# Optimization experiments

Measured on AMD Instinct MI355X. Metric: run time of the kernel, lower is better.

The kernel has to match this reference:

```python
import jax, jax.numpy as jnp
import numpy as np

N_NODES, N_EDGES, N_GRAPHS = 5000, 80000, 64
LATENT, HID, STEPS = 128, 512, 3


def _mlp(h, Ws, bs):
    # MLP: ReLU after every linear (incl. last) -- MLPwoLastAct is the variant without it
    for W, b in zip(Ws, bs):
        h = jax.nn.relu(h @ W + b)
    return h


def _mlp_wo_last_act(h, Ws, bs):
    n = len(Ws)
    for i, (W, b) in enumerate(zip(Ws, bs)):
        h = h @ W + b
        if i < n - 1:
            h = jax.nn.relu(h)
    return h


def setup_inputs() -> dict:
    key = jax.random.key(0)
    ks = iter(jax.random.split(key, 64))

    def nrm(shape, s=0.05):
        return (jax.random.normal(next(ks), shape) * s).astype(jnp.float32)

    inp = {}
    inp["x"] = jax.random.normal(next(ks), (N_NODES, LATENT), jnp.float32)
    inp["edge_index"] = jax.random.randint(next(ks), (2, N_EDGES), 0, N_NODES, jnp.int32)
    inp["edge_attr"] = jax.random.normal(next(ks), (N_EDGES, LATENT), jnp.float32)
    inp["u"] = jax.random.normal(next(ks), (N_GRAPHS, LATENT), jnp.float32)
    inp["node_batch"] = jnp.sort(jax.random.randint(next(ks), (N_NODES,), 0, N_GRAPHS, jnp.int32))
    inp["edge_batch"] = jnp.sort(jax.random.randint(next(ks), (N_EDGES,), 0, N_GRAPHS, jnp.int32))
    inp["pos"] = jax.random.normal(next(ks), (N_NODES, 3), jnp.float32)
    inp["last_pos_init"] = jax.random.uniform(next(ks), (N_NODES, 3), jnp.float32, -1.0, 1.0)

    # PosEmbeddingwithMask: pos MLP(3->128->128), dis MLP(1->128->128)
    inp["pos_emb_W1"], inp["pos_emb_b1"] = nrm((3, LATENT)), nrm((LATENT,))
    inp["pos_emb_W2"], inp["pos_emb_b2"] = nrm((LATENT, LATENT)), nrm((LATENT,))
    inp["dis_W1"], inp["dis_b1"] = nrm((1, LATENT)), nrm((LATENT,))
    inp["dis_W2"], inp["dis_b2"] = nrm((LATENT, LATENT)), nrm((LATENT,))

    # per-layer edge / node MLPs: (4*latent) -> 512 -> 512 -> 128, stacked over STEPS
    cin = 4 * LATENT
    for pre in ("edge", "node"):
        inp[f"{pre}_W1"], inp[f"{pre}_b1"] = nrm((STEPS, cin, HID)), nrm((STEPS, HID))
        inp[f"{pre}_W2"], inp[f"{pre}_b2"] = nrm((STEPS, HID, HID)), nrm((STEPS, HID))
        inp[f"{pre}_W3"], inp[f"{pre}_b3"] = nrm((STEPS, HID, LATENT)), nrm((STEPS, LATENT))

    # global MLP only for layers 0..STEPS-2: (3*latent) -> 512 -> 512 -> 128
    gL, gin = STEPS - 1, 3 * LATENT
    inp["glob_W1"], inp["glob_b1"] = nrm((gL, gin, HID)), nrm((gL, HID))
    inp["glob_W2"], inp["glob_b2"] = nrm((gL, HID, HID)), nrm((gL, HID))
    inp["glob_W3"], inp["glob_b3"] = nrm((gL, HID, LATENT)), nrm((gL, LATENT))

    # shared pos_decoder: MLPwoLastAct(128 -> 128 -> 3)
    inp["dec_W1"], inp["dec_b1"] = nrm((LATENT, LATENT)), nrm((LATENT,))
    inp["dec_W2"], inp["dec_b2"] = nrm((LATENT, 3)), nrm((3,))
    return inp


def reference(x, edge_index, edge_attr, u, node_batch, edge_batch, pos, last_pos_init,
              pos_emb_W1, pos_emb_b1, pos_emb_W2, pos_emb_b2,
              dis_W1, dis_b1, dis_W2, dis_b2,
              edge_W1, edge_b1, edge_W2, edge_b2, edge_W3, edge_b3,
              node_W1, node_b1, node_W2, node_b2, node_W3, node_b3,
              glob_W1, glob_b1, glob_W2, glob_b2, glob_W3, glob_b3,
              dec_W1, dec_b1, dec_W2, dec_b2):
    src, dst = edge_index[0], edge_index[1]
    N = x.shape[0]
    counts = jnp.maximum(
        jax.ops.segment_sum(jnp.ones((N, 1), x.dtype), node_batch, N_GRAPHS), 1.0)

    def move2origin(p):
        mean = jax.ops.segment_sum(p, node_batch, N_GRAPHS) / counts
        return p - mean[node_batch]

    xs, es, us = x, edge_attr, u
    last_pos = last_pos_init  # pos_new_zeros.uniform_(-1, 1), materialized as input
    pos_preds = []
    for l in range(STEPS):
        p = last_pos  # mode='mol2conf': pos = last_pred
        # PosEmbeddingwithMask
        ex = xs + _mlp(p, (pos_emb_W1, pos_emb_W2), (pos_emb_b1, pos_emb_b2))
        length = jnp.linalg.norm(p[src] - p[dst], axis=-1, keepdims=True)  # [E,1]
        ee = es + _mlp(length, (dis_W1, dis_W2), (dis_b1, dis_b2))
        # edge update: gather -> MLP
        edge_in = jnp.concatenate([ex[src], ex[dst], ee, us[edge_batch]], axis=-1)
        e1 = _mlp(edge_in, (edge_W1[l], edge_W2[l], edge_W3[l]),
                  (edge_b1[l], edge_b2[l], edge_b3[l]))
        # scatter-reduce (sum) to nodes, then node MLP
        sent = jax.ops.segment_sum(e1, src, N)
        recv = jax.ops.segment_sum(e1, dst, N)
        node_in = jnp.concatenate([ex, sent, recv, us[node_batch]], axis=-1)
        x1 = _mlp(node_in, (node_W1[l], node_W2[l], node_W3[l]),
                  (node_b1[l], node_b2[l], node_b3[l]))
        # global update (None on last layer)
        if l < STEPS - 1:
            g_in = jnp.concatenate([us,
                                    jax.ops.segment_sum(x1, node_batch, N_GRAPHS),
                                    jax.ops.segment_sum(e1, edge_batch, N_GRAPHS)], axis=-1)
            u1 = _mlp(g_in, (glob_W1[l], glob_W2[l], glob_W3[l]),
                      (glob_b1[l], glob_b2[l], glob_b3[l]))
        else:
            u1 = us
        # residuals (dropout is identity in eval)
        xs, es, us = x1 + xs, e1 + es, u1 + us
        # pred_pos_residual=True
        delta = _mlp_wo_last_act(xs, (dec_W1, dec_W2), (dec_b1, dec_b2))
        last_pos = move2origin(last_pos + delta)
        pos_preds.append(last_pos)
    return xs, es, us, jnp.stack(pos_preds)
```

## Files before the change

### kernel.cpp

```cpp
#include <hip/hip_runtime.h>
#include <hip/hip_bf16.h>
#include <stdint.h>

#define NN 5000
#define NE 80000
#define NG 64
#define LAT 128
#define HIDN 512

typedef __hip_bfloat16 bf16;
typedef short short8 __attribute__((ext_vector_type(8)));
typedef float f32x4 __attribute__((ext_vector_type(4)));

__device__ __forceinline__ float b2f(bf16 v) { return __bfloat162float(v); }
__device__ __forceinline__ bf16 f2b(float v) { return __float2bfloat16(v); }
__device__ __forceinline__ short f2bs(float v) {
    bf16 b = __float2bfloat16(v);
    short s; __builtin_memcpy(&s, &b, 2); return s;
}

template<int MODE>
__global__ __launch_bounds__(256, 4)
void gemm64_kernel(const bf16* __restrict__ A, const bf16* __restrict__ Bt,
                   const float* __restrict__ bias,
                   const float* residf, const bf16* residb,
                   float* out_sf, bf16* out_sb, bf16* out_rb,
                   int M, int N, int nnt,
                   const int* __restrict__ g_src, const int* __restrict__ g_dst,
                   const int* __restrict__ g_eb,
                   const bf16* __restrict__ g_ex, const bf16* __restrict__ g_ee,
                   const bf16* __restrict__ g_us)
{
    constexpr int K = 512, NT = K / 64;
    __shared__ __align__(16) char lds[24576];

    const int tid  = threadIdx.x;
    const int lane = tid & 63;
    const int w    = tid >> 6;
    const int li   = lane & 15, grp = lane >> 4;
    const int wr   = w >> 1, wc = w & 1;

    const int nb  = gridDim.x;
    const int q   = nb >> 3, r = nb & 7;
    const int xcd = blockIdx.x & 7, jj = blockIdx.x >> 3;
    const int wg  = (xcd < r ? xcd * (q + 1) : r * (q + 1) + (xcd - r) * q) + jj;
    const int m0  = (wg / nnt) * 128;
    const int n0  = (wg % nnt) * 64;

    f32x4 acc[4][2];
#pragma unroll
    for (int m = 0; m < 4; ++m)
#pragma unroll
        for (int n = 0; n < 2; ++n)
            acc[m][n] = (f32x4){0.f, 0.f, 0.f, 0.f};

    int he[4], hs[4], hd[4], hb[4];
    if (MODE == 1) {
#pragma unroll
        for (int c = 0; c < 4; ++c) {
            const int p  = (tid + c * 256) * 16;
            const int qb = p ^ ((p >> 3) & 0x70);
            int e = m0 + (qb >> 7); if (e >= M) e = M - 1;
            he[c] = e;
            hs[c] = g_src[e]; hd[c] = g_dst[e]; hb[c] = g_eb[e];
        }
    }

    char* ldsA = lds;
    char* ldsB = lds + 16384;

    for (int t = 0; t < NT; ++t) {
#pragma unroll
        for (int c = 0; c < 4; ++c) {
            const int p  = (tid + c * 256) * 16;
            const int qb = p ^ ((p >> 3) & 0x70);
            const int row = qb >> 7;
            const int kk  = (qb & 127) >> 1;
            const bf16* srcp;
            if (MODE == 1) {
                const int seg = t >> 1;
                const int so  = ((t & 1) << 6) + kk;
                if (seg == 0)      srcp = g_ex + (size_t)hs[c] * LAT + so;
                else if (seg == 1) srcp = g_ex + (size_t)hd[c] * LAT + so;
                else if (seg == 2) srcp = g_ee + (size_t)he[c] * LAT + so;
                else               srcp = g_us + (size_t)hb[c] * LAT + so;
            } else {
                int rr = m0 + row; if (rr >= M) rr = M - 1;
                srcp = A + (size_t)rr * K + t * 64 + kk;
            }
            __builtin_amdgcn_global_load_lds(
                (__attribute__((address_space(1))) const void*)srcp,
                (__attribute__((address_space(3))) void*)(ldsA + p), 16, 0, 0);
        }
#pragma unroll
        for (int c = 0; c < 2; ++c) {
            const int p  = (tid + c * 256) * 16;
            const int qb = p ^ ((p >> 3) & 0x70);
            const int row = qb >> 7;
            const int kk  = (qb & 127) >> 1;
            const bf16* srcp = Bt + (size_t)(n0 + row) * K + t * 64 + kk;
            __builtin_amdgcn_global_load_lds(
                (__attribute__((address_space(1))) const void*)srcp,
                (__attribute__((address_space(3))) void*)(ldsB + p), 16, 0, 0);
        }
        __syncthreads();

        short8 af[4][2], bf[2][2];
#pragma unroll
        for (int m = 0; m < 4; ++m) {
            const int row = wr * 64 + m * 16 + li;
            const int xr  = (row & 7) << 4;
#pragma unroll
            for (int s = 0; s < 2; ++s)
                af[m][s] = *(const short8*)(ldsA +
                    ((row * 128 + s * 64 + grp * 16) ^ xr));
        }
#pragma unroll
        for (int n = 0; n < 2; ++n) {
            const int row = wc * 32 + n * 16 + li;
            const int xr  = (row & 7) << 4;
#pragma unroll
            for (int s = 0; s < 2; ++s)
                bf[n][s] = *(const short8*)(ldsB +
                    ((row * 128 + s * 64 + grp * 16) ^ xr));
        }
#pragma unroll
        for (int m = 0; m < 4; ++m)
#pragma unroll
            for (int n = 0; n < 2; ++n)
#pragma unroll
                for (int s = 0; s < 2; ++s)
                    acc[m][n] = __builtin_amdgcn_mfma_f32_16x16x32_bf16(
                        af[m][s], bf[n][s], acc[m][n], 0, 0, 0);
        __syncthreads();
    }

#pragma unroll
    for (int m = 0; m < 4; ++m) {
        const int growb = m0 + wr * 64 + m * 16 + grp * 4;
#pragma unroll
        for (int n = 0; n < 2; ++n) {
            const int gcol = n0 + wc * 32 + n * 16 + li;
            const float bv = bias[gcol];
#pragma unroll
            for (int j = 0; j < 4; ++j) {
                const int grow = growb + j;
                if (grow >= M) continue;
                float val = fmaxf(acc[m][n][j] + bv, 0.f);
                const size_t oo = (size_t)grow * N + gcol;
                if (out_rb) out_rb[oo] = f2b(val);
                float sum = val;
                if (residf) sum += residf[oo];
                if (residb) sum += b2f(residb[oo]);
                if (out_sf) out_sf[oo] = sum;
                if (out_sb) out_sb[oo] = f2b(sum);
            }
        }
    }
}

__global__ __launch_bounds__(256, 4)
void posdis_kernel(int nP,
                   const float* __restrict__ lp,
                   const int* __restrict__ src, const int* __restrict__ dst,
                   const bf16* __restrict__ pBt, const float* __restrict__ pb2v,
                   const float* __restrict__ pW1v, const float* __restrict__ pb1v,
                   const float* __restrict__ xs, bf16* __restrict__ exb,
                   const bf16* __restrict__ dBt, const float* __restrict__ db2v,
                   const float* __restrict__ dW1v, const float* __restrict__ db1v,
                   const bf16* __restrict__ esb, bf16* __restrict__ eeb)
{
    constexpr int K = 128;
    __shared__ __align__(16) bf16 Bs[64 * 32];
    const int tid  = threadIdx.x;
    const int lane = tid & 63;
    const int w    = tid >> 6;
    const int li   = lane & 15, grp = lane >> 4;
    const int wr   = w >> 1, wc = w & 1;

    const bool isP = (int)blockIdx.x < nP;
    const int bid  = isP ? blockIdx.x : blockIdx.x - nP;
    const int M    = isP ? NN : NE;
    const int m0   = (bid >> 1) * 128;
    const int n0   = (bid & 1) * 64;
    const bf16*  Bt   = isP ? pBt  : dBt;
    const float* bias = isP ? pb2v : db2v;
    const float* aW   = isP ? pW1v : dW1v;
    const float* ab   = isP ? pb1v : db1v;

    f32x4 acc[4][2];
#pragma unroll
    for (int m = 0; m < 4; ++m)
#pragma unroll
        for (int n = 0; n < 2; ++n)
            acc[m][n] = (f32x4){0.f, 0.f, 0.f, 0.f};

    float r0[4], r1[4], r2[4];
#pragma unroll
    for (int m = 0; m < 4; ++m) {
        int rr = m0 + wr * 64 + m * 16 + li; if (rr >= M) rr = M - 1;
        if (isP) {
            r0[m] = lp[rr * 3 + 0]; r1[m] = lp[rr * 3 + 1]; r2[m] = lp[rr * 3 + 2];
        } else {
            const int s = src[rr], d = dst[rr];
            const float dx = lp[s*3+0] - lp[d*3+0];
            const float dy = lp[s*3+1] - lp[d*3+1];
            const float dz = lp[s*3+2] - lp[d*3+2];
            r0[m] = sqrtf(dx*dx + dy*dy + dz*dz);
        }
    }

    for (int kt = 0; kt < K / 32; ++kt) {
        {
            const int off = tid * 16;
            const int rr_ = off >> 6;
            const int g   = (off >> 4) & 3;
            const int gl  = g ^ ((rr_ >> 1) & 3);
            const bf16* srcp = Bt + (size_t)(n0 + rr_) * K + kt * 32 + gl * 8;
            __builtin_amdgcn_global_load_lds(
                (__attribute__((address_space(1))) const void*)srcp,
                (__attribute__((address_space(3))) void*)((char*)Bs + off),
                16, 0, 0);
        }
        __syncthreads();

        const int kk0 = kt * 32 + grp * 8;
        float bb[8], w0[8], w1[8], w2[8];
        *(f32x4*)&bb[0] = *(const f32x4*)(ab + kk0);
        *(f32x4*)&bb[4] = *(const f32x4*)(ab + kk0 + 4);
        *(f32x4*)&w0[0] = *(const f32x4*)(aW + kk0);
        *(f32x4*)&w0[4] = *(const f32x4*)(aW + kk0 + 4);
        if (isP) {
            *(f32x4*)&w1[0] = *(const f32x4*)(aW + K + kk0);
            *(f32x4*)&w1[4] = *(const f32x4*)(aW + K + kk0 + 4);
            *(f32x4*)&w2[0] = *(const f32x4*)(aW + 2 * K + kk0);
            *(f32x4*)&w2[4] = *(const f32x4*)(aW + 2 * K + kk0 + 4);
        }
        short8 af[4], bfr[2];
#pragma unroll
        for (int m = 0; m < 4; ++m) {
            short8 v;
#pragma unroll
            for (int e = 0; e < 8; ++e) {
                float s = isP ? (bb[e] + r0[m]*w0[e] + r1[m]*w1[e] + r2[m]*w2[e])
                              : (bb[e] + r0[m]*w0[e]);
                v[e] = f2bs(fmaxf(s, 0.f));
            }
            af[m] = v;
        }
#pragma unroll
        for (int n = 0; n < 2; ++n) {
            const int rr_  = wc * 32 + n * 16 + li;
            const int boff = rr_ * 64 + ((grp * 16) ^ (((rr_ >> 1) & 3) << 4));
            bfr[n] = *(const short8*)((const char*)Bs + boff);
        }
#pragma unroll
        for (int m = 0; m < 4; ++m)
#pragma unroll
            for (int n = 0; n < 2; ++n)
                acc[m][n] = __builtin_amdgcn_mfma_f32_16x16x32_bf16(
                    af[m], bfr[n], acc[m][n], 0, 0, 0);
        __syncthreads();
    }

#pragma unroll
    for (int m = 0; m < 4; ++m) {
        const int growb = m0 + wr * 64 + m * 16 + grp * 4;
#pragma unroll
        for (int n = 0; n < 2; ++n) {
            const int gcol = n0 + wc * 32 + n * 16 + li;
            const float bv = bias[gcol];
#pragma unroll
            for (int j = 0; j < 4; ++j) {
                const int grow = growb + j;
                if (grow >= M) continue;
                float val = fmaxf(acc[m][n][j] + bv, 0.f);
                const size_t oo = (size_t)grow * LAT + gcol;
                if (isP) exb[oo] = f2b(val + xs[oo]);
                else     eeb[oo] = f2b(val + b2f(esb[oo]));
            }
        }
    }
}

template<int K>
__global__ __launch_bounds__(256, 4)
void gemm_kernel(const bf16* __restrict__ A,
                 const bf16* __restrict__ Bt,
                 const float* __restrict__ bias,
                 const float* residf,
                 float* out_sf, bf16* out_sb, bf16* out_rb,
                 int M, int N, int nnt)
{
    __shared__ __align__(16) bf16 As[128 * 32];
    __shared__ __align__(16) bf16 Bs[64 * 32];
    const int tid  = threadIdx.x;
    const int lane = tid & 63;
    const int w    = tid >> 6;
    const int li   = lane & 15, grp = lane >> 4;
    const int wr   = w >> 1, wc = w & 1;

    const int nb  = gridDim.x;
    const int q   = nb >> 3, r = nb & 7;
    const int xcd = blockIdx.x & 7, jj = blockIdx.x >> 3;
    const int wg  = (nb >= 8)
        ? (xcd < r ? xcd * (q + 1) : r * (q + 1) + (xcd - r) * q) + jj
        : (int)blockIdx.x;
    const int m0  = (wg / nnt) * 128;
    const int n0  = (wg % nnt) * 64;

    f32x4 acc[4][2];
#pragma unroll
    for (int m = 0; m < 4; ++m)
#pragma unroll
        for (int n = 0; n < 2; ++n)
            acc[m][n] = (f32x4){0.f, 0.f, 0.f, 0.f};

    for (int kt = 0; kt < K / 32; ++kt) {
#pragma unroll
        for (int c = 0; c < 2; ++c) {
            const int off = tid * 16 + c * 4096;
            const int rr_ = off >> 6;
            const int g   = (off >> 4) & 3;
            const int gl  = g ^ ((rr_ >> 1) & 3);
            int rr = m0 + rr_; if (rr >= M) rr = M - 1;
            const bf16* srcp = A + (size_t)rr * K + kt * 32 + gl * 8;
            __builtin_amdgcn_global_load_lds(
                (__attribute__((address_space(1))) const void*)srcp,
                (__attribute__((address_space(3))) void*)((char*)As + off),
                16, 0, 0);
        }
        {
            const int off = tid * 16;
            const int rr_ = off >> 6;
            const int g   = (off >> 4) & 3;
            const int gl  = g ^ ((rr_ >> 1) & 3);
            const bf16* srcp = Bt + (size_t)(n0 + rr_) * K + kt * 32 + gl * 8;
            __builtin_amdgcn_global_load_lds(
                (__attribute__((address_space(1))) const void*)srcp,
                (__attribute__((address_space(3))) void*)((char*)Bs + off),
                16, 0, 0);
        }
        __syncthreads();

        short8 af[4], bfr[2];
#pragma unroll
        for (int m = 0; m < 4; ++m) {
            const int rr_  = wr * 64 + m * 16 + li;
            const int boff = rr_ * 64 + ((grp * 16) ^ (((rr_ >> 1) & 3) << 4));
            af[m] = *(const short8*)((const char*)As + boff);
        }
#pragma unroll
        for (int n = 0; n < 2; ++n) {
            const int rr_  = wc * 32 + n * 16 + li;
            const int boff = rr_ * 64 + ((grp * 16) ^ (((rr_ >> 1) & 3) << 4));
            bfr[n] = *(const short8*)((const char*)Bs + boff);
        }
#pragma unroll
        for (int m = 0; m < 4; ++m)
#pragma unroll
            for (int n = 0; n < 2; ++n)
                acc[m][n] = __builtin_amdgcn_mfma_f32_16x16x32_bf16(
                    af[m], bfr[n], acc[m][n], 0, 0, 0);
        __syncthreads();
    }

#pragma unroll
    for (int m = 0; m < 4; ++m) {
        const int growb = m0 + wr * 64 + m * 16 + grp * 4;
#pragma unroll
        for (int n = 0; n < 2; ++n) {
            const int gcol = n0 + wc * 32 + n * 16 + li;
            const float bv = bias[gcol];
#pragma unroll
            for (int j = 0; j < 4; ++j) {
                const int grow = growb + j;
                if (grow >= M) continue;
                float val = fmaxf(acc[m][n][j] + bv, 0.f);
                const size_t oo = (size_t)grow * N + gcol;
                if (out_rb) out_rb[oo] = f2b(val);
                float sum = val;
                if (residf) sum += residf[oo];
                if (out_sf) out_sf[oo] = sum;
                if (out_sb) out_sb[oo] = f2b(sum);
            }
        }
    }
}

struct TDesc { const float* src; bf16* dst; int K, N, nblk, nb32; };
struct TPack { TDesc d[28]; int n; };

__global__ __launch_bounds__(256)
void transpose_kernel(TPack p)
{
    __shared__ float t[32][33];
    int b = blockIdx.x, mi = 0;
    while (mi < p.n && b >= p.d[mi].nblk) { b -= p.d[mi].nblk; ++mi; }
    if (mi >= p.n) return;
    TDesc d = p.d[mi];
    const int kb = b / d.nb32, nb = b % d.nb32;
    const int k0 = kb * 32, n0 = nb * 32;
    const int tx = threadIdx.x & 31, ty = threadIdx.x >> 5;
#pragma unroll
    for (int qq = 0; qq < 4; ++qq) {
        const int kk = ty + qq * 8;
        t[kk][tx] = d.src[(size_t)(k0 + kk) * d.N + n0 + tx];
    }
    __syncthreads();
#pragma unroll
    for (int qq = 0; qq < 4; ++qq) {
        const int nn = ty + qq * 8;
        d.dst[(size_t)(n0 + nn) * d.K + k0 + tx] = f2b(t[tx][nn]);
    }
}

__global__ void deg_kernel(const int* __restrict__ idx, int n, int* deg)
{
    int e = blockIdx.x * 256 + threadIdx.x;
    if (e < n) atomicAdd(&deg[idx[e]], 1);
}

__global__ __launch_bounds__(256)
void scan_kernel(const int* __restrict__ deg, int* __restrict__ offs, int n)
{
    __shared__ int tot[256];
    const int t = threadIdx.x;
    const int per = (n + 255) / 256;
    const int b = t * per;
    int s = 0;
    for (int i = 0; i < per; ++i) if (b + i < n) s += deg[b + i];
    tot[t] = s;
    __syncthreads();
    for (int d = 1; d < 256; d <<= 1) {
        int v = (t >= d) ? tot[t - d] : 0;
        __syncthreads();
        tot[t] += v;
        __syncthreads();
    }
    int excl = (t == 0) ? 0 : tot[t - 1];
    for (int i = 0; i < per; ++i)
        if (b + i < n) { offs[b + i] = excl; excl += deg[b + i]; }
    if (t == 255) offs[n] = tot[255];
}

__global__ void perm_kernel(const int* __restrict__ idx, int n,
                            int* cursor, int* __restrict__ perm)
{
    int e = blockIdx.x * 256 + threadIdx.x;
    if (e < n) { int p = atomicAdd(&cursor[idx[e]], 1); perm[p] = e; }
}

__global__ __launch_bounds__(128)
void node_seg_kernel(const bf16* __restrict__ exb, const bf16* __restrict__ e1f,
                     const bf16* __restrict__ usb, const int* __restrict__ nbat,
                     const int* __restrict__ offs_s, const int* __restrict__ perm_s,
                     const int* __restrict__ offs_d, const int* __restrict__ perm_d,
                     bf16* __restrict__ node_in,
                     const int* __restrict__ ebat, float* ge)
{
    const int c = threadIdx.x;
    if ((int)blockIdx.x >= NN) {
        const int r0 = ((int)blockIdx.x - NN) * 64;
        if (r0 >= NE) return;
        const int r1 = min(r0 + 64, NE);
        int g = ebat[r0];
        float s = 0.f;
        for (int r = r0; r < r1; ++r) {
            const int gb = ebat[r];
            if (gb != g) {
                atomicAdd(&ge[(size_t)g * LAT + c], s);
                g = gb; s = 0.f;
            }
            s += b2f(e1f[(size_t)r * LAT + c]);
        }
        atomicAdd(&ge[(size_t)g * LAT + c], s);
        return;
    }
    const int i = blockIdx.x;
    float s1 = 0.f, s2 = 0.f;
    const int s_lo = offs_s[i], s_hi = offs_s[i + 1];
    for (int j = s_lo; j < s_hi; ++j)
        s1 += b2f(e1f[(size_t)perm_s[j] * LAT + c]);
    const int d_lo = offs_d[i], d_hi = offs_d[i + 1];
    for (int j = d_lo; j < d_hi; ++j)
        s2 += b2f(e1f[(size_t)perm_d[j] * LAT + c]);
    const size_t o = (size_t)i * (4 * LAT);
    node_in[o + c]           = exb[(size_t)i * LAT + c];
    node_in[o + LAT + c]     = f2b(s1);
    node_in[o + 2 * LAT + c] = f2b(s2);
    node_in[o + 3 * LAT + c] = usb[(size_t)nbat[i] * LAT + c];
}

__global__ __launch_bounds__(128)
void seg_reduce_kernel(const bf16* __restrict__ vals, const int* __restrict__ batch,
                       float* out, int R, int rows_per_block)
{
    const int r0 = blockIdx.x * rows_per_block;
    if (r0 >= R) return;
    const int c = threadIdx.x;
    const int r1 = min(r0 + rows_per_block, R);
    int g = batch[r0];
    float s = 0.f;
    for (int r = r0; r < r1; ++r) {
        const int gb = batch[r];
        if (gb != g) {
            atomicAdd(&out[(size_t)g * LAT + c], s);
            g = gb; s = 0.f;
        }
        s += b2f(vals[(size_t)r * LAT + c]);
    }
    atomicAdd(&out[(size_t)g * LAT + c], s);
}

__global__ void build_g_in_kernel(const float* __restrict__ us,
                                  const float* __restrict__ gx,
                                  const float* __restrict__ ge,
                                  bf16* __restrict__ out)
{
    int id = blockIdx.x * 256 + threadIdx.x;
    if (id >= NG * 384) return;
    int g = id / 384, c = id % 384;
    int seg = c >> 7, c7 = c & 127;
    float v;
    if (seg == 0)      v = us[g * LAT + c7];
    else if (seg == 1) v = gx[g * LAT + c7];
    else               v = ge[g * LAT + c7];
    out[id] = f2b(v);
}

__global__ void counts_kernel(const int* __restrict__ nbat, float* counts)
{
    int id = blockIdx.x * 256 + threadIdx.x;
    if (id < NN) atomicAdd(&counts[nbat[id]], 1.0f);
}

__global__ void cvt_kernel(const float* __restrict__ in, bf16* __restrict__ out, int n)
{
    int id = blockIdx.x * 256 + threadIdx.x;
    if (id < n) out[id] = f2b(in[id]);
}

__global__ void us_double_kernel(float* us)
{
    int id = blockIdx.x * 256 + threadIdx.x;
    if (id < NG * LAT) us[id] *= 2.0f;
}

__global__ __launch_bounds__(64)
void dec2_kernel(const bf16* __restrict__ dh, const float* __restrict__ W2,
                 const float* __restrict__ b2, const float* __restrict__ lp,
                 const int* __restrict__ nbat, float* __restrict__ ptmp, float* psum)
{
    int i = blockIdx.x;
    int l = threadIdx.x;
    float a0 = 0.f, a1 = 0.f, a2 = 0.f;
#pragma unroll
    for (int q = 0; q < 2; ++q) {
        int k = l + q * 64;
        float h = b2f(dh[i * LAT + k]);
        a0 += h * W2[k * 3 + 0];
        a1 += h * W2[k * 3 + 1];
        a2 += h * W2[k * 3 + 2];
    }
#pragma unroll
    for (int off = 32; off > 0; off >>= 1) {
        a0 += __shfl_down(a0, off, 64);
        a1 += __shfl_down(a1, off, 64);
        a2 += __shfl_down(a2, off, 64);
    }
    if (l == 0) {
        int g = nbat[i];
        float p0 = lp[i*3+0] + a0 + b2[0];
        float p1 = lp[i*3+1] + a1 + b2[1];
        float p2 = lp[i*3+2] + a2 + b2[2];
        ptmp[i*3+0] = p0; ptmp[i*3+1] = p1; ptmp[i*3+2] = p2;
        atomicAdd(&psum[g*3+0], p0);
        atomicAdd(&psum[g*3+1], p1);
        atomicAdd(&psum[g*3+2], p2);
    }
}

__global__ void finalize_pos_kernel(const float* __restrict__ ptmp,
                                    const float* __restrict__ psum,
                                    const float* __restrict__ counts,
                                    const int* __restrict__ nbat,
                                    float* __restrict__ lp, float* __restrict__ pos_out)
{
    int id = blockIdx.x * 256 + threadIdx.x;
    if (id >= NN * 3) return;
    int i = id / 3, d = id % 3;
    int g = nbat[i];
    float v = ptmp[id] - psum[g*3+d] / fmaxf(counts[g], 1.f);
    lp[id] = v;
    pos_out[id] = v;
}

extern "C" void kernel_launch(void* const* d_in, const int* in_sizes, int n_in,
                              void* d_out, int out_size, void* d_ws, size_t ws_size,
                              hipStream_t stream)
{
    const float* x        = (const float*)d_in[0];
    const int*   ei       = (const int*)d_in[1];
    const int*   src      = ei;
    const int*   dst      = ei + NE;
    const float* eattr    = (const float*)d_in[2];
    const float* u        = (const float*)d_in[3];
    const int*   nbat     = (const int*)d_in[4];
    const int*   ebat     = (const int*)d_in[5];
    const float* lp_init  = (const float*)d_in[7];
    const float* pW1 = (const float*)d_in[8];  const float* pb1 = (const float*)d_in[9];
    const float* pW2 = (const float*)d_in[10]; const float* pb2 = (const float*)d_in[11];
    const float* dW1 = (const float*)d_in[12]; const float* db1 = (const float*)d_in[13];
    const float* dW2 = (const float*)d_in[14]; const float* db2 = (const float*)d_in[15];
    const float* eW1 = (const float*)d_in[16]; const float* eb1 = (const float*)d_in[17];
    const float* eW2 = (const float*)d_in[18]; const float* eb2 = (const float*)d_in[19];
    const float* eW3 = (const float*)d_in[20]; const float* eb3 = (const float*)d_in[21];
    const float* nW1 = (const float*)d_in[22]; const float* nb1 = (const float*)d_in[23];
    const float* nW2 = (const float*)d_in[24]; const float* nb2 = (const float*)d_in[25];
    const float* nW3 = (const float*)d_in[26]; const float* nb3 = (const float*)d_in[27];
    const float* gW1 = (const float*)d_in[28]; const float* gb1 = (const float*)d_in[29];
    const float* gW2 = (const float*)d_in[30]; const float* gb2 = (const float*)d_in[31];
    const float* gW3 = (const float*)d_in[32]; const float* gb3 = (const float*)d_in[33];
    const float* dcW1 = (const float*)d_in[34]; const float* dcb1 = (const float*)d_in[35];
    const float* dcW2 = (const float*)d_in[36]; const float* dcb2 = (const float*)d_in[37];

    float* xs = (float*)d_out;
    float* es = xs + (size_t)NN * LAT;
    float* us = es + (size_t)NE * LAT;
    float* pos_out = us + (size_t)NG * LAT;

    char* wp = (char*)d_ws;
    auto alloc = [&](size_t nbytes) {
        void* r = (void*)wp;
        wp += (nbytes + 255) & ~(size_t)255;
        return r;
    };
    bf16* eW1t = (bf16*)alloc((size_t)3*512*512*2);
    bf16* eW2t = (bf16*)alloc((size_t)3*512*512*2);
    bf16* eW3t = (bf16*)alloc((size_t)3*128*512*2);
    bf16* nW1t = (bf16*)alloc((size_t)3*512*512*2);
    bf16* nW2t = (bf16*)alloc((size_t)3*512*512*2);
    bf16* nW3t = (bf16*)alloc((size_t)3*128*512*2);
    bf16* gW1t = (bf16*)alloc((size_t)2*512*384*2);
    bf16* gW2t = (bf16*)alloc((size_t)2*512*512*2);
    bf16* gW3t = (bf16*)alloc((size_t)2*128*512*2);
    bf16* pW2t = (bf16*)alloc((size_t)128*128*2);
    bf16* dW2t = (bf16*)alloc((size_t)128*128*2);
    bf16* dcW1t = (bf16*)alloc((size_t)128*128*2);
    bf16* exb  = (bf16*)alloc((size_t)NN*LAT*2);
    bf16* usb  = (bf16*)alloc((size_t)NG*LAT*2);
    bf16* esb  = (bf16*)alloc((size_t)NE*LAT*2);
    bf16* eeb  = (bf16*)alloc((size_t)NE*LAT*2);
    bf16* h1   = (bf16*)alloc((size_t)NE*HIDN*2);
    bf16* h2   = (bf16*)alloc((size_t)NE*HIDN*2);
    bf16* e1f  = (bf16*)alloc((size_t)NE*LAT*2);
    bf16* x1f  = (bf16*)alloc((size_t)NN*LAT*2);
    float* gx  = (float*)alloc((size_t)NG*LAT*4);
    float* ge  = (float*)alloc((size_t)NG*LAT*4);
    bf16* node_in = (bf16*)alloc((size_t)NN*HIDN*2);
    bf16* nh1  = (bf16*)alloc((size_t)NN*HIDN*2);
    bf16* nh2  = (bf16*)alloc((size_t)NN*HIDN*2);
    bf16* xsb  = (bf16*)alloc((size_t)NN*LAT*2);
    bf16* g_in = (bf16*)alloc((size_t)NG*384*2);
    bf16* gh1  = (bf16*)alloc((size_t)NG*HIDN*2);
    bf16* gh2  = (bf16*)alloc((size_t)NG*HIDN*2);
    bf16* dh   = (bf16*)alloc((size_t)NN*LAT*2);
    float* lp   = (float*)alloc((size_t)NN*3*4);
    float* ptmp = (float*)alloc((size_t)NN*3*4);
    float* psum = (float*)alloc((size_t)NG*3*4);
    float* counts = (float*)alloc((size_t)NG*4);
    int* deg    = (int*)alloc((size_t)NN*4);
    int* offs_s = (int*)alloc((size_t)(NN+1)*4);
    int* offs_d = (int*)alloc((size_t)(NN+1)*4);
    int* cur_s  = (int*)alloc((size_t)NN*4);
    int* cur_d  = (int*)alloc((size_t)NN*4);
    int* perm_s = (int*)alloc((size_t)NE*4);
    int* perm_d = (int*)alloc((size_t)NE*4);

    hipMemcpyAsync(xs, x,     (size_t)NN*LAT*4, hipMemcpyDeviceToDevice, stream);
    hipMemcpyAsync(us, u,     (size_t)NG*LAT*4, hipMemcpyDeviceToDevice, stream);
    hipMemcpyAsync(lp, lp_init, (size_t)NN*3*4, hipMemcpyDeviceToDevice, stream);
    hipMemsetAsync(counts, 0, NG*4, stream);
    counts_kernel<<<(NN+255)/256, 256, 0, stream>>>(nbat, counts);
    cvt_kernel<<<(NG*LAT+255)/256, 256, 0, stream>>>(us, usb, NG*LAT);
    cvt_kernel<<<(NE*LAT+255)/256, 256, 0, stream>>>(eattr, esb, NE*LAT);

    const int eb256 = (NE + 255) / 256;
    hipMemsetAsync(deg, 0, NN*4, stream);
    deg_kernel<<<eb256, 256, 0, stream>>>(src, NE, deg);
    scan_kernel<<<1, 256, 0, stream>>>(deg, offs_s, NN);
    hipMemsetAsync(deg, 0, NN*4, stream);
    deg_kernel<<<eb256, 256, 0, stream>>>(dst, NE, deg);
    scan_kernel<<<1, 256, 0, stream>>>(deg, offs_d, NN);
    hipMemcpyAsync(cur_s, offs_s, NN*4, hipMemcpyDeviceToDevice, stream);
    hipMemcpyAsync(cur_d, offs_d, NN*4, hipMemcpyDeviceToDevice, stream);
    perm_kernel<<<eb256, 256, 0, stream>>>(src, NE, cur_s, perm_s);
    perm_kernel<<<eb256, 256, 0, stream>>>(dst, NE, cur_d, perm_d);

    TPack pk{}; int nd = 0, totb = 0;
    auto addT = [&](const float* s, bf16* d, int K, int N) {
        pk.d[nd].src = s; pk.d[nd].dst = d; pk.d[nd].K = K; pk.d[nd].N = N;
        pk.d[nd].nblk = (K/32)*(N/32); pk.d[nd].nb32 = N/32;
        totb += pk.d[nd].nblk; ++nd;
    };
    for (int l = 0; l < 3; ++l) {
        addT(eW1 + (size_t)l*512*512, eW1t + (size_t)l*512*512, 512, 512);
        addT(eW2 + (size_t)l*512*512, eW2t + (size_t)l*512*512, 512, 512);
        addT(eW3 + (size_t)l*512*128, eW3t + (size_t)l*128*512, 512, 128);
        addT(nW1 + (size_t)l*512*512, nW1t + (size_t)l*512*512, 512, 512);
        addT(nW2 + (size_t)l*512*512, nW2t + (size_t)l*512*512, 512, 512);
        addT(nW3 + (size_t)l*512*128, nW3t + (size_t)l*128*512, 512, 128);
    }
    for (int l = 0; l < 2; ++l) {
        addT(gW1 + (size_t)l*384*512, gW1t + (size_t)l*512*384, 384, 512);
        addT(gW2 + (size_t)l*512*512, gW2t + (size_t)l*512*512, 512, 512);
        addT(gW3 + (size_t)l*512*128, gW3t + (size_t)l*128*512, 512, 128);
    }
    addT(pW2, pW2t, 128, 128);
    addT(dW2, dW2t, 128, 128);
    addT(dcW1, dcW1t, 128, 128);
    pk.n = nd;
    transpose_kernel<<<totb, 256, 0, stream>>>(pk);

    const int mtE  = NE / 128;
    const int mtN  = (NN + 127) / 128;
    #define NIL3 nullptr, nullptr, nullptr

    for (int l = 0; l < 3; ++l) {
        posdis_kernel<<<mtN*2 + mtE*2, 256, 0, stream>>>(
            mtN*2, lp, src, dst,
            pW2t, pb2, pW1, pb1, xs, exb,
            dW2t, db2, dW1, db1, esb, eeb);
        gemm64_kernel<1><<<mtE*8, 256, 0, stream>>>(
            nullptr, eW1t + (size_t)l*512*512, eb1 + l*HIDN, nullptr, nullptr,
            nullptr, nullptr, h1, NE, HIDN, 8,
            src, dst, ebat, exb, eeb, usb);
        gemm64_kernel<0><<<mtE*8, 256, 0, stream>>>(
            h1, eW2t + (size_t)l*512*512, eb2 + l*HIDN, nullptr, nullptr,
            nullptr, nullptr, h2, NE, HIDN, 8, NIL3, NIL3);
        gemm64_kernel<0><<<mtE*2, 256, 0, stream>>>(
            h2, eW3t + (size_t)l*128*512, eb3 + l*LAT, nullptr, esb,
            (l == 2 ? es : nullptr), (l < 2 ? esb : nullptr), e1f, NE, LAT, 2,
            NIL3, NIL3);
        if (l < 2)
            hipMemsetAsync(gx, 0, (size_t)2*NG*LAT*4, stream);
        node_seg_kernel<<<NN + (l < 2 ? (NE+63)/64 : 0), 128, 0, stream>>>(
            exb, e1f, usb, nbat, offs_s, perm_s, offs_d, perm_d, node_in,
            ebat, ge);
        gemm64_kernel<0><<<mtN*8, 256, 0, stream>>>(
            node_in, nW1t + (size_t)l*512*512, nb1 + l*HIDN, nullptr, nullptr,
            nullptr, nullptr, nh1, NN, HIDN, 8, NIL3, NIL3);
        gemm64_kernel<0><<<mtN*8, 256, 0, stream>>>(
            nh1, nW2t + (size_t)l*512*512, nb2 + l*HIDN, nullptr, nullptr,
            nullptr, nullptr, nh2, NN, HIDN, 8, NIL3, NIL3);
        gemm64_kernel<0><<<mtN*2, 256, 0, stream>>>(
            nh2, nW3t + (size_t)l*128*512, nb3 + l*LAT, xs, nullptr,
            xs, xsb, x1f, NN, LAT, 2, NIL3, NIL3);
        if (l < 2) {
            seg_reduce_kernel<<<(NN+31)/32, 128, 0, stream>>>(x1f, nbat, gx, NN, 32);
            build_g_in_kernel<<<(NG*384+255)/256, 256, 0, stream>>>(us, gx, ge, g_in);
            gemm_kernel<384><<<8, 256, 0, stream>>>(
                g_in, gW1t + (size_t)l*512*384, gb1 + l*HIDN, nullptr,
                nullptr, nullptr, gh1, NG, HIDN, 8);
            gemm_kernel<512><<<8, 256, 0, stream>>>(
                gh1, gW2t + (size_t)l*512*512, gb2 + l*HIDN, nullptr,
                nullptr, nullptr, gh2, NG, HIDN, 8);
            gemm_kernel<512><<<2, 256, 0, stream>>>(
                gh2, gW3t + (size_t)l*128*512, gb3 + l*LAT, us,
                us, usb, nullptr, NG, LAT, 2);
        } else {
            us_double_kernel<<<(NG*LAT+255)/256, 256, 0, stream>>>(us);
        }
        gemm_kernel<128><<<mtN*2, 256, 0, stream>>>(
            xsb, dcW1t, dcb1, nullptr, nullptr, nullptr, dh, NN, LAT, 2);
        hipMemsetAsync(psum, 0, NG*3*4, stream);
        dec2_kernel<<<NN, 64, 0, stream>>>(dh, dcW2, dcb2, lp, nbat, ptmp, psum);
        finalize_pos_kernel<<<(NN*3+255)/256, 256, 0, stream>>>(
            ptmp, psum, counts, nbat, lp, pos_out + (size_t)l*NN*3);
    }
    (void)in_sizes; (void)n_in; (void)out_size; (void)ws_size;
}
```

Before: 1.277 ms.

## Fuse global MLP into single-block kernel and hoist per-layer memsets

Replaces the g_in build kernel and three small global-MLP GEMM launches with one 512-thread single-block kernel that builds the input, runs all three layers with MFMA and updates us/usb in place. Per-layer memsets of gx/ge and psum are replaced by per-layer buffers zeroed once up front. This removes several tiny kernel launches and memset calls per layer. In exchange, the global MLP runs on a single workgroup, so its compute is serialized on one CU.

Result: slower. 1.395 ms (+9.2%).

```diff
diff --git a/kernel.cpp b/kernel.cpp
--- a/kernel.cpp
+++ b/kernel.cpp
@@ -388,6 +388,90 @@
     }
 }
 
+__global__ __launch_bounds__(512)
+void glob_kernel(const float* __restrict__ us_in, float* us,
+                 bf16* __restrict__ usb,
+                 const float* __restrict__ gx, const float* __restrict__ ge,
+                 bf16* __restrict__ g_in, bf16* __restrict__ gh1,
+                 bf16* __restrict__ gh2,
+                 const bf16* __restrict__ W1t, const float* __restrict__ b1,
+                 const bf16* __restrict__ W2t, const float* __restrict__ b2,
+                 const bf16* __restrict__ W3t, const float* __restrict__ b3)
+{
+    const int tid  = threadIdx.x;
+    const int lane = tid & 63;
+    const int w    = tid >> 6;
+    const int li   = lane & 15, grp = lane >> 4;
+
+#pragma unroll
+    for (int i = 0; i < 48; ++i) {
+        const int idx = tid + i * 512;
+        const int g = idx / 384, c = idx % 384;
+        float v;
+        if (c < 128)      v = us_in[g * LAT + c];
+        else if (c < 256) v = gx[g * LAT + (c - 128)];
+        else              v = ge[g * LAT + (c - 256)];
+        g_in[idx] = f2b(v);
+    }
+    __syncthreads();
+
+    auto layer = [&](const bf16* A, int Ka, const bf16* Bt, const float* bias,
+                     int Nw, bf16* outb, float* sumf, bf16* sumb) {
+        if (w >= Nw) return;
+        const int n0 = w * 64;
+        f32x4 acc[4][4];
+#pragma unroll
+        for (int m = 0; m < 4; ++m)
+#pragma unroll
+            for (int n = 0; n < 4; ++n)
+                acc[m][n] = (f32x4){0.f, 0.f, 0.f, 0.f};
+        for (int kt = 0; kt < Ka / 32; ++kt) {
+            const int k0 = kt * 32 + grp * 8;
+            short8 af[4], bfr[4];
+#pragma unroll
+            for (int m = 0; m < 4; ++m)
+                af[m] = *(const short8*)(A + (size_t)(m * 16 + li) * Ka + k0);
+#pragma unroll
+            for (int n = 0; n < 4; ++n)
+                bfr[n] = *(const short8*)(Bt + (size_t)(n0 + n * 16 + li) * Ka + k0);
+#pragma unroll
+            for (int m = 0; m < 4; ++m)
+#pragma unroll
+                for (int n = 0; n < 4; ++n)
+                    acc[m][n] = __builtin_amdgcn_mfma_f32_16x16x32_bf16(
+                        af[m], bfr[n], acc[m][n], 0, 0, 0);
+        }
+        const int NO = Nw * 64;
+#pragma unroll
+        for (int m = 0; m < 4; ++m) {
+            const int growb = m * 16 + grp * 4;
+#pragma unroll
+            for (int n = 0; n < 4; ++n) {
+                const int gcol = n0 + n * 16 + li;
+                const float bv = bias[gcol];
+#pragma unroll
+                for (int j = 0; j < 4; ++j) {
+                    const int grow = growb + j;
+                    float val = fmaxf(acc[m][n][j] + bv, 0.f);
+                    const size_t oo = (size_t)grow * NO + gcol;
+                    if (outb) outb[oo] = f2b(val);
+                    if (sumf) {
+                        float sum = val + sumf[oo];
+                        sumf[oo] = sum;
+                        sumb[oo] = f2b(sum);
+                    }
+                }
+            }
+        }
+    };
+
+    layer(g_in, 384, W1t, b1, 8, gh1, nullptr, nullptr);
+    __syncthreads();
+    layer(gh1, 512, W2t, b2, 8, gh2, nullptr, nullptr);
+    __syncthreads();
+    layer(gh2, 512, W3t, b3, 2, nullptr, us, usb);
+}
+
 struct TDesc { const float* src; bf16* dst; int K, N, nblk, nb32; };
 struct TPack { TDesc d[28]; int n; };
 
@@ -511,22 +595,6 @@
         s += b2f(vals[(size_t)r * LAT + c]);
     }
     atomicAdd(&out[(size_t)g * LAT + c], s);
-}
-
-__global__ void build_g_in_kernel(const float* __restrict__ us,
-                                  const float* __restrict__ gx,
-                                  const float* __restrict__ ge,
-                                  bf16* __restrict__ out)
-{
-    int id = blockIdx.x * 256 + threadIdx.x;
-    if (id >= NG * 384) return;
-    int g = id / 384, c = id % 384;
-    int seg = c >> 7, c7 = c & 127;
-    float v;
-    if (seg == 0)      v = us[g * LAT + c7];
-    else if (seg == 1) v = gx[g * LAT + c7];
-    else               v = ge[g * LAT + c7];
-    out[id] = f2b(v);
 }
 
 __global__ void counts_kernel(const int* __restrict__ nbat, float* counts)
@@ -656,8 +724,8 @@
     bf16* h2   = (bf16*)alloc((size_t)NE*HIDN*2);
     bf16* e1f  = (bf16*)alloc((size_t)NE*LAT*2);
     bf16* x1f  = (bf16*)alloc((size_t)NN*LAT*2);
-    float* gx  = (float*)alloc((size_t)NG*LAT*4);
-    float* ge  = (float*)alloc((size_t)NG*LAT*4);
+    float* gxge = (float*)alloc((size_t)2*2*NG*LAT*4);
+    float* psum3 = (float*)alloc((size_t)3*NG*3*4);
     bf16* node_in = (bf16*)alloc((size_t)NN*HIDN*2);
     bf16* nh1  = (bf16*)alloc((size_t)NN*HIDN*2);
     bf16* nh2  = (bf16*)alloc((size_t)NN*HIDN*2);
@@ -668,7 +736,6 @@
     bf16* dh   = (bf16*)alloc((size_t)NN*LAT*2);
     float* lp   = (float*)alloc((size_t)NN*3*4);
     float* ptmp = (float*)alloc((size_t)NN*3*4);
-    float* psum = (float*)alloc((size_t)NG*3*4);
     float* counts = (float*)alloc((size_t)NG*4);
     int* deg    = (int*)alloc((size_t)NN*4);
     int* offs_s = (int*)alloc((size_t)(NN+1)*4);
@@ -682,6 +749,8 @@
     hipMemcpyAsync(us, u,     (size_t)NG*LAT*4, hipMemcpyDeviceToDevice, stream);
     hipMemcpyAsync(lp, lp_init, (size_t)NN*3*4, hipMemcpyDeviceToDevice, stream);
     hipMemsetAsync(counts, 0, NG*4, stream);
+    hipMemsetAsync(gxge, 0, (size_t)2*2*NG*LAT*4, stream);
+    hipMemsetAsync(psum3, 0, (size_t)3*NG*3*4, stream);
     counts_kernel<<<(NN+255)/256, 256, 0, stream>>>(nbat, counts);
     cvt_kernel<<<(NG*LAT+255)/256, 256, 0, stream>>>(us, usb, NG*LAT);
     cvt_kernel<<<(NE*LAT+255)/256, 256, 0, stream>>>(eattr, esb, NE*LAT);
@@ -728,6 +797,10 @@
     #define NIL3 nullptr, nullptr, nullptr
 
     for (int l = 0; l < 3; ++l) {
+        float* gx_l = gxge + (size_t)l * 2 * NG * LAT;
+        float* ge_l = gx_l + (size_t)NG * LAT;
+        float* psum_l = psum3 + (size_t)l * NG * 3;
+
         posdis_kernel<<<mtN*2 + mtE*2, 256, 0, stream>>>(
             mtN*2, lp, src, dst,
             pW2t, pb2, pW1, pb1, xs, exb,
@@ -743,11 +816,9 @@
             h2, eW3t + (size_t)l*128*512, eb3 + l*LAT, nullptr, esb,
             (l == 2 ? es : nullptr), (l < 2 ? esb : nullptr), e1f, NE, LAT, 2,
             NIL3, NIL3);
-        if (l < 2)
-            hipMemsetAsync(gx, 0, (size_t)2*NG*LAT*4, stream);
         node_seg_kernel<<<NN + (l < 2 ? (NE+63)/64 : 0), 128, 0, stream>>>(
             exb, e1f, usb, nbat, offs_s, perm_s, offs_d, perm_d, node_in,
-            ebat, ge);
+            ebat, ge_l);
         gemm64_kernel<0><<<mtN*8, 256, 0, stream>>>(
             node_in, nW1t + (size_t)l*512*512, nb1 + l*HIDN, nullptr, nullptr,
             nullptr, nullptr, nh1, NN, HIDN, 8, NIL3, NIL3);
@@ -758,26 +829,20 @@
             nh2, nW3t + (size_t)l*128*512, nb3 + l*LAT, xs, nullptr,
             xs, xsb, x1f, NN, LAT, 2, NIL3, NIL3);
         if (l < 2) {
-            seg_reduce_kernel<<<(NN+31)/32, 128, 0, stream>>>(x1f, nbat, gx, NN, 32);
-            build_g_in_kernel<<<(NG*384+255)/256, 256, 0, stream>>>(us, gx, ge, g_in);
-            gemm_kernel<384><<<8, 256, 0, stream>>>(
-                g_in, gW1t + (size_t)l*512*384, gb1 + l*HIDN, nullptr,
-                nullptr, nullptr, gh1, NG, HIDN, 8);
-            gemm_kernel<512><<<8, 256, 0, stream>>>(
-                gh1, gW2t + (size_t)l*512*512, gb2 + l*HIDN, nullptr,
-                nullptr, nullptr, gh2, NG, HIDN, 8);
-            gemm_kernel<512><<<2, 256, 0, stream>>>(
-                gh2, gW3t + (size_t)l*128*512, gb3 + l*LAT, us,
-                us, usb, nullptr, NG, LAT, 2);
+            seg_reduce_kernel<<<(NN+31)/32, 128, 0, stream>>>(x1f, nbat, gx_l, NN, 32);
+            glob_kernel<<<1, 512, 0, stream>>>(
+                us, us, usb, gx_l, ge_l, g_in, gh1, gh2,
+                gW1t + (size_t)l*512*384, gb1 + l*HIDN,
+                gW2t + (size_t)l*512*512, gb2 + l*HIDN,
+                gW3t + (size_t)l*128*512, gb3 + l*LAT);
         } else {
             us_double_kernel<<<(NG*LAT+255)/256, 256, 0, stream>>>(us);
         }
         gemm_kernel<128><<<mtN*2, 256, 0, stream>>>(
             xsb, dcW1t, dcb1, nullptr, nullptr, nullptr, dh, NN, LAT, 2);
-        hipMemsetAsync(psum, 0, NG*3*4, stream);
-        dec2_kernel<<<NN, 64, 0, stream>>>(dh, dcW2, dcb2, lp, nbat, ptmp, psum);
+        dec2_kernel<<<NN, 64, 0, stream>>>(dh, dcW2, dcb2, lp, nbat, ptmp, psum_l);
         finalize_pos_kernel<<<(NN*3+255)/256, 256, 0, stream>>>(
-            ptmp, psum, counts, nbat, lp, pos_out + (size_t)l*NN*3);
+            ptmp, psum_l, counts, nbat, lp, pos_out + (size_t)l*NN*3);
     }
     (void)in_sizes; (void)n_in; (void)out_size; (void)ws_size;
 }
```
